# Optimization experiments

Hardware: AMD Instinct MI355X
Metric: run time of the kernel (lower is better)

## Reference

```python
import jax, jax.numpy as jnp
import numpy as np

B, L = 64, 512          # graphs, nodes per graph
N = B * L               # total nodes
INPUT_DIM, D, H, LAYERS, OUT = 128, 128, 8, 6, 10
DH = D // H
FF = 4 * D
E = 4 * N
SCALE = 0.02


def setup_inputs() -> dict:
    key = jax.random.key(0)
    ks = jax.random.split(key, 12)
    p = {}
    p['x'] = jax.random.normal(ks[0], (N, INPUT_DIM), jnp.float32)
    p['edge_index'] = jax.random.randint(ks[1], (2, E), 0, N, dtype=jnp.int64)
    p['batch'] = jnp.repeat(jnp.arange(B, dtype=jnp.int32), L)  # sorted graph ids
    p['max_nodes'] = L
    p['Wp'] = jax.random.normal(ks[2], (INPUT_DIM, D), jnp.float32) * SCALE
    p['bp'] = jnp.zeros((D,), jnp.float32)
    p['qkv_w'] = jax.random.normal(ks[3], (LAYERS, 3 * D, D), jnp.float32) * SCALE
    p['qkv_b'] = jnp.zeros((LAYERS, 3 * D), jnp.float32)
    p['out_w'] = jax.random.normal(ks[4], (LAYERS, D, D), jnp.float32) * SCALE
    p['out_b'] = jnp.zeros((LAYERS, D), jnp.float32)
    p['ln1_g'] = jnp.ones((LAYERS, D), jnp.float32)
    p['ln1_b'] = jnp.zeros((LAYERS, D), jnp.float32)
    p['ffn_w1'] = jax.random.normal(ks[5], (LAYERS, D, FF), jnp.float32) * SCALE
    p['ffn_b1'] = jnp.zeros((LAYERS, FF), jnp.float32)
    p['ffn_w2'] = jax.random.normal(ks[6], (LAYERS, FF, D), jnp.float32) * SCALE
    p['ffn_b2'] = jnp.zeros((LAYERS, D), jnp.float32)
    p['ln2_g'] = jnp.ones((LAYERS, D), jnp.float32)
    p['ln2_b'] = jnp.zeros((LAYERS, D), jnp.float32)
    p['cls_w1'] = jax.random.normal(ks[7], (D, D // 2), jnp.float32) * SCALE
    p['cls_b1'] = jnp.zeros((D // 2,), jnp.float32)
    p['cls_w2'] = jax.random.normal(ks[8], (D // 2, OUT), jnp.float32) * SCALE
    p['cls_b2'] = jnp.zeros((OUT,), jnp.float32)
    return p


def _ln(x, g, b, eps=1e-5):
    m = x.mean(-1, keepdims=True)
    v = ((x - m) ** 2).mean(-1, keepdims=True)
    return (x - m) * jax.lax.rsqrt(v + eps) * g + b


def _forward(x, batch, max_nodes, Wp, bp, qkv_w, qkv_b, out_w, out_b,
             ln1_g, ln1_b, ffn_w1, ffn_b1, ffn_w2, ffn_b2, ln2_g, ln2_b,
             cls_w1, cls_b1, cls_w2, cls_b2):
    n = x.shape[0]
    # --- vectorized ragged-to-dense (replaces the per-graph python loop) ---
    ones = jnp.ones((n,), jnp.int32)
    counts = jax.ops.segment_sum(ones, batch, num_segments=B)          # [B]
    starts = jnp.concatenate([jnp.zeros((1,), jnp.int32), jnp.cumsum(counts)[:-1]])
    pos = jnp.arange(n, dtype=jnp.int32) - starts[batch]               # slot within graph
    h0 = x @ Wp + bp                                                   # [N, D]
    h = jnp.zeros((B, max_nodes, D), h0.dtype).at[batch, pos].set(h0)  # [B, L, D]
    mask = jnp.zeros((B, max_nodes), bool).at[batch, pos].set(True)    # [B, L]
    # additive key-padding bias (src_key_padding_mask=~mask)
    bias = jnp.where(mask, 0.0, -1e9)[:, None, None, :]                # [B,1,1,L]
    inv_sqrt = 1.0 / np.sqrt(DH)
    for i in range(LAYERS):
        # --- post-norm MHA block ---
        qkv = jnp.einsum('bld,ed->ble', h, qkv_w[i]) + qkv_b[i]        # [B,L,3D]
        q, k, v = jnp.split(qkv, 3, axis=-1)
        q = q.reshape(B, max_nodes, H, DH).transpose(0, 2, 1, 3)       # [B,H,L,dh]
        k = k.reshape(B, max_nodes, H, DH).transpose(0, 2, 1, 3)
        v = v.reshape(B, max_nodes, H, DH).transpose(0, 2, 1, 3)
        scores = jnp.einsum('bhqd,bhkd->bhqk', q, k) * inv_sqrt + bias
        attn = jax.nn.softmax(scores, axis=-1)
        o = jnp.einsum('bhqk,bhkd->bhqd', attn, v)                     # [B,H,L,dh]
        o = o.transpose(0, 2, 1, 3).reshape(B, max_nodes, D)
        o = jnp.einsum('bld,ed->ble', o, out_w[i]) + out_b[i]
        h = _ln(h + o, ln1_g[i], ln1_b[i])
        # --- FFN block ---
        ff = jax.nn.relu(h @ ffn_w1[i] + ffn_b1[i]) @ ffn_w2[i] + ffn_b2[i]
        h = _ln(h + ff, ln2_g[i], ln2_b[i])
    # --- masked mean pooling per graph ---
    denom = jnp.maximum(counts.astype(h.dtype), 1.0)[:, None]          # [B,1]
    pooled = (h * mask[..., None].astype(h.dtype)).sum(axis=1) / denom # [B,D]
    # --- classifier head ---
    hid = jax.nn.relu(pooled @ cls_w1 + cls_b1)
    return hid @ cls_w2 + cls_b2                                       # [B,OUT]


def reference(x, edge_index, batch, max_nodes, Wp, bp, qkv_w, qkv_b, out_w, out_b,
              ln1_g, ln1_b, ffn_w1, ffn_b1, ffn_w2, ffn_b2, ln2_g, ln2_b,
              cls_w1, cls_b1, cls_w2, cls_b2):
    # edge_index is accepted (as in the torch module) but never used.
    return _forward(x, batch, max_nodes, Wp, bp, qkv_w, qkv_b, out_w, out_b,
                    ln1_g, ln1_b, ffn_w1, ffn_b1, ffn_w2, ffn_b2, ln2_g, ln2_b,
                    cls_w1, cls_b1, cls_w2, cls_b2)
```

## Files before the change

### kernel.cpp

```cpp
#include <hip/hip_runtime.h>
#include <hip/hip_bf16.h>


#define NROWS (64 * 512)
#define NLAYER 6

typedef __bf16 bf16x8 __attribute__((ext_vector_type(8)));
typedef float  f32x4  __attribute__((ext_vector_type(4)));
typedef float  f32x16 __attribute__((ext_vector_type(16)));

#define QSCALE 0.36067376022224085f

#if defined(__has_builtin)
#  if __has_builtin(__builtin_amdgcn_exp2f)
#    define FAST_EXP2(x) __builtin_amdgcn_exp2f(x)
#  endif
#endif
#ifndef FAST_EXP2
#  define FAST_EXP2(x) __expf((x) * 0.6931471805599453f)
#endif

__device__ __forceinline__ __hip_bfloat16 f2bf(float x) { return __float2bfloat16(x); }

__device__ __forceinline__ __hip_bfloat16 bf_rta(float a) {
  union { float f; unsigned u; } c{a};
  return __builtin_bit_cast(__hip_bfloat16, (unsigned short)((c.u + 0x8000u) >> 16));
}
__device__ __forceinline__ unsigned pk_rta(float a, float b) {
  union { float f; unsigned u; } ca{a}, cb{b};
  return ((ca.u + 0x8000u) >> 16) | ((cb.u + 0x8000u) & 0xFFFF0000u);
}
__device__ __forceinline__ float bf_hi(unsigned u) {
  return __builtin_bit_cast(float, u & 0xFFFF0000u);
}
__device__ __forceinline__ float bf_lo(unsigned u) {
  return __builtin_bit_cast(float, u << 16);
}

#define PN_X   (NROWS * 128)
#define PN_WP  (128 * 128)
#define PN_QW  (6 * 384 * 128)
#define PN_QB  (6 * 384)
#define PN_OW  (6 * 128 * 128)
#define PN_W1  (6 * 128 * 512)
#define PN_W2  (6 * 512 * 128)
#define PB1 PN_X
#define PB2 (PB1 + PN_WP)
#define PB3 (PB2 + PN_QW)
#define PB4 (PB3 + PN_QB)
#define PB5 (PB4 + PN_OW)
#define PB6 (PB5 + PN_W1)
#define PB7 (PB6 + PN_W2)

__global__ __launch_bounds__(256) void prep_kernel(
    const float* __restrict__ x, __hip_bfloat16* __restrict__ xb,
    const float* __restrict__ Wp, __hip_bfloat16* __restrict__ wp_t,
    const float* __restrict__ qkv_w, __hip_bfloat16* __restrict__ qkvw,
    const float* __restrict__ qkv_b, float* __restrict__ qb_s,
    const float* __restrict__ out_w, __hip_bfloat16* __restrict__ outw,
    const float* __restrict__ ffn_w1, __hip_bfloat16* __restrict__ w1t,
    const float* __restrict__ ffn_w2, __hip_bfloat16* __restrict__ w2t)
{
  const int idx = blockIdx.x * 256 + threadIdx.x;
  if (idx < PB1) {
    xb[idx] = f2bf(x[idx]);
  } else if (idx < PB2) {
    const int i = idx - PB1;
    const int c = i >> 7, r = i & 127;
    wp_t[i] = f2bf(Wp[r * 128 + c]);
  } else if (idx < PB3) {
    const int i = idx - PB2;
    const int row = (i >> 7) % 384;
    qkvw[i] = f2bf(qkv_w[i] * ((row < 128) ? QSCALE : 1.f));
  } else if (idx < PB4) {
    const int i = idx - PB3;
    qb_s[i] = qkv_b[i] * (((i % 384) < 128) ? QSCALE : 1.f);
  } else if (idx < PB5) {
    const int i = idx - PB4;
    outw[i] = f2bf(out_w[i]);
  } else if (idx < PB6) {
    const int i = idx - PB5;
    const int l = i >> 16, j = i & 65535;
    const int c = j >> 7, r = j & 127;
    w1t[i] = f2bf(ffn_w1[l * 65536 + r * 512 + c]);
  } else if (idx < PB7) {
    const int i = idx - PB6;
    const int l = i >> 16, j = i & 65535;
    const int c = j >> 9, r = j & 511;
    w2t[i] = f2bf(ffn_w2[l * 65536 + r * 128 + c]);
  }
}

__global__ __launch_bounds__(256) void gemm_fk(
    const __hip_bfloat16* __restrict__ A, const __hip_bfloat16* __restrict__ B,
    const float* __restrict__ bias, __hip_bfloat16* __restrict__ outb,
    __hip_bfloat16* __restrict__ hb,
    const float* __restrict__ lng, const float* __restrict__ lnb,
    int M, int K, int flags)
{
  __shared__ __align__(16) __hip_bfloat16 As[64 * 136];
  __shared__ __align__(16) __hip_bfloat16 Bs[128 * 136];

  const int tid = threadIdx.x;
  const int m0 = blockIdx.x << 6;
  const int wave = tid >> 6;
  const int lane = tid & 63;
  const int quad = lane >> 4;
  const int l15 = lane & 15;
  const int wrow = wave * 16;

  f32x4 acc[8];
#pragma unroll
  for (int ni = 0; ni < 8; ++ni) acc[ni] = (f32x4){0.f, 0.f, 0.f, 0.f};

  for (int kc = 0; kc < K; kc += 128) {
#pragma unroll
    for (int p = 0; p < 4; ++p) {
      const int e = tid + (p << 8);
      const int row = e >> 4;
      const int c = e & 15;
      *(uint4*)&As[row * 136 + c * 8] =
          *(const uint4*)(A + (size_t)(m0 + row) * K + kc + c * 8);
    }
#pragma unroll
    for (int p = 0; p < 8; ++p) {
      const int e = tid + (p << 8);
      const int row = e >> 4;
      const int c = e & 15;
      *(uint4*)&Bs[row * 136 + c * 8] =
          *(const uint4*)(B + (size_t)row * K + kc + c * 8);
    }
    __syncthreads();

#pragma unroll
    for (int ks = 0; ks < 4; ++ks) {
      const bf16x8 af = *(const bf16x8*)&As[(wrow + l15) * 136 + ks * 32 + quad * 8];
#pragma unroll
      for (int ni = 0; ni < 8; ++ni) {
        const bf16x8 bfr =
            *(const bf16x8*)&Bs[(ni * 16 + l15) * 136 + ks * 32 + quad * 8];
        acc[ni] = __builtin_amdgcn_mfma_f32_16x16x32_bf16(af, bfr, acc[ni], 0, 0, 0);
      }
    }
    if (kc + 128 < K) __syncthreads();
  }

  if (flags & 2) {
#pragma unroll
    for (int r = 0; r < 4; ++r) {
      const size_t row = (size_t)(m0 + wrow + quad * 4 + r);
      float s = 0.f, sq = 0.f;
#pragma unroll
      for (int ni = 0; ni < 8; ++ni) {
        const int cl = ni * 16 + l15;
        const float v = acc[ni][r] + bias[cl] +
                        __bfloat162float(hb[row * 128 + cl]);
        acc[ni][r] = v;
        s += v;
        sq += v * v;
      }
#pragma unroll
      for (int off = 1; off <= 8; off <<= 1) {
        s += __shfl_xor(s, off, 64);
        sq += __shfl_xor(sq, off, 64);
      }
      const float mean = s * (1.f / 128.f);
      const float var = sq * (1.f / 128.f) - mean * mean;
      const float rs = rsqrtf(var + 1e-5f);
#pragma unroll
      for (int ni = 0; ni < 8; ++ni) {
        const int cl = ni * 16 + l15;
        const float o = (acc[ni][r] - mean) * rs * lng[cl] + lnb[cl];
        hb[row * 128 + cl] = bf_rta(o);
      }
    }
  } else {
#pragma unroll
    for (int ni = 0; ni < 8; ++ni) {
      const int cl = ni * 16 + l15;
      const float bv = bias[cl];
#pragma unroll
      for (int r = 0; r < 4; ++r) {
        float v = acc[ni][r] + bv;
        if (flags & 1) v = fmaxf(v, 0.f);
        outb[(size_t)(m0 + wrow + quad * 4 + r) * 128 + cl] = bf_rta(v);
      }
    }
  }
}

__global__ __launch_bounds__(256) void oproj_ffn(
    const __hip_bfloat16* __restrict__ ab,
    __hip_bfloat16* __restrict__ hb,
    const __hip_bfloat16* __restrict__ ow,
    const float* __restrict__ ob,
    const float* __restrict__ ln1g, const float* __restrict__ ln1b,
    const __hip_bfloat16* __restrict__ w1,
    const __hip_bfloat16* __restrict__ w2,
    const float* __restrict__ fb1, const float* __restrict__ fb2,
    const float* __restrict__ ln2g, const float* __restrict__ ln2b)
{
  __shared__ __align__(16) __hip_bfloat16 AF[64 * 136];
  __shared__ __align__(16) __hip_bfloat16 Bs[128 * 136];

  const int tid = threadIdx.x;
  const int m0 = blockIdx.x << 6;
  const int wave = tid >> 6;
  const int lane = tid & 63;
  const int quad = lane >> 4;
  const int l15 = lane & 15;
  const int wrow = wave * 16;
  const int node = m0 + wrow + l15;
  const int ch0 = quad * 4;

  uint2 hres[8];
#pragma unroll
  for (int ni = 0; ni < 8; ++ni)
    hres[ni] = *(const uint2*)(hb + (size_t)node * 128 + ni * 16 + ch0);

#pragma unroll
  for (int p = 0; p < 4; ++p) {
    const int e = tid + (p << 8);
    const int row = e >> 4, c = e & 15;
    *(uint4*)&AF[row * 136 + c * 8] =
        *(const uint4*)(ab + (size_t)(m0 + row) * 128 + c * 8);
  }
#pragma unroll
  for (int p = 0; p < 8; ++p) {
    const int e = tid + (p << 8);
    const int row = e >> 4, c = e & 15;
    *(uint4*)&Bs[row * 136 + c * 8] =
        *(const uint4*)(ow + (size_t)row * 128 + c * 8);
  }
  __syncthreads();

  bf16x8 af[4];
#pragma unroll
  for (int ks = 0; ks < 4; ++ks)
    af[ks] = *(const bf16x8*)&AF[(wrow + l15) * 136 + ks * 32 + quad * 8];

  f32x4 acc[8];
#pragma unroll
  for (int ni = 0; ni < 8; ++ni) acc[ni] = (f32x4){0.f, 0.f, 0.f, 0.f};
#pragma unroll
  for (int ks = 0; ks < 4; ++ks)
#pragma unroll
    for (int ni = 0; ni < 8; ++ni) {
      const bf16x8 bfr =
          *(const bf16x8*)&Bs[(ni * 16 + l15) * 136 + ks * 32 + quad * 8];
      acc[ni] = __builtin_amdgcn_mfma_f32_16x16x32_bf16(bfr, af[ks], acc[ni], 0, 0, 0);
    }

  {
    float s = 0.f, sq = 0.f;
#pragma unroll
    for (int ni = 0; ni < 8; ++ni) {
      const f32x4 obv = *(const f32x4*)(ob + ni * 16 + ch0);
#pragma unroll
      for (int r = 0; r < 4; ++r) {
        const unsigned hu = (r & 2) ? hres[ni].y : hres[ni].x;
        const float hv = (r & 1) ? bf_hi(hu) : bf_lo(hu);
        const float v = acc[ni][r] + obv[r] + hv;
        acc[ni][r] = v;
        s += v;
        sq += v * v;
      }
    }
    s += __shfl_xor(s, 16, 64);  sq += __shfl_xor(sq, 16, 64);
    s += __shfl_xor(s, 32, 64);  sq += __shfl_xor(sq, 32, 64);
    const float mean = s * (1.f / 128.f);
    const float rs = rsqrtf(sq * (1.f / 128.f) - mean * mean + 1e-5f);
#pragma unroll
    for (int ni = 0; ni < 8; ++ni) {
      const f32x4 gv = *(const f32x4*)(ln1g + ni * 16 + ch0);
      const f32x4 bv = *(const f32x4*)(ln1b + ni * 16 + ch0);
      const float o0 = (acc[ni][0] - mean) * rs * gv[0] + bv[0];
      const float o1 = (acc[ni][1] - mean) * rs * gv[1] + bv[1];
      const float o2 = (acc[ni][2] - mean) * rs * gv[2] + bv[2];
      const float o3 = (acc[ni][3] - mean) * rs * gv[3] + bv[3];
      const uint2 pk = make_uint2(pk_rta(o0, o1), pk_rta(o2, o3));
      hres[ni] = pk;
      *(uint2*)&AF[(wrow + l15) * 136 + ni * 16 + ch0] = pk;
    }
  }

  __syncthreads();
#pragma unroll
  for (int p = 0; p < 8; ++p) {
    const int e = tid + (p << 8);
    const int row = e >> 4, cc = e & 15;
    *(uint4*)&Bs[row * 136 + cc * 8] =
        *(const uint4*)(w1 + (size_t)row * 128 + cc * 8);
  }
  bf16x8 hf[4];
#pragma unroll
  for (int ks = 0; ks < 4; ++ks)
    hf[ks] = *(const bf16x8*)&AF[(wrow + l15) * 136 + ks * 32 + quad * 8];
  __syncthreads();

  f32x4 facc[8];
#pragma unroll
  for (int ni = 0; ni < 8; ++ni) facc[ni] = (f32x4){0.f, 0.f, 0.f, 0.f};

  for (int c = 0; c < 4; ++c) {
    if (c > 0) {
      __syncthreads();
#pragma unroll
      for (int p = 0; p < 8; ++p) {
        const int e = tid + (p << 8);
        const int row = e >> 4, cc = e & 15;
        *(uint4*)&Bs[row * 136 + cc * 8] =
            *(const uint4*)(w1 + (size_t)(c * 128 + row) * 128 + cc * 8);
      }
      __syncthreads();
    }

    f32x4 fc[8];
#pragma unroll
    for (int ni = 0; ni < 8; ++ni) fc[ni] = (f32x4){0.f, 0.f, 0.f, 0.f};
#pragma unroll
    for (int ks = 0; ks < 4; ++ks)
#pragma unroll
      for (int ni = 0; ni < 8; ++ni) {
        const bf16x8 wf =
            *(const bf16x8*)&Bs[(ni * 16 + l15) * 136 + ks * 32 + quad * 8];
        fc[ni] = __builtin_amdgcn_mfma_f32_16x16x32_bf16(wf, hf[ks], fc[ni], 0, 0, 0);
      }
#pragma unroll
    for (int ni = 0; ni < 8; ++ni) {
      const f32x4 bv = *(const f32x4*)(fb1 + c * 128 + ni * 16 + ch0);
      const float v0 = fmaxf(fc[ni][0] + bv[0], 0.f);
      const float v1 = fmaxf(fc[ni][1] + bv[1], 0.f);
      const float v2 = fmaxf(fc[ni][2] + bv[2], 0.f);
      const float v3 = fmaxf(fc[ni][3] + bv[3], 0.f);
      *(uint2*)&AF[(wrow + l15) * 136 + ni * 16 + ch0] =
          make_uint2(pk_rta(v0, v1), pk_rta(v2, v3));
    }
    __syncthreads();

#pragma unroll
    for (int p = 0; p < 8; ++p) {
      const int e = tid + (p << 8);
      const int row = e >> 4, cc = e & 15;
      *(uint4*)&Bs[row * 136 + cc * 8] =
          *(const uint4*)(w2 + (size_t)row * 512 + c * 128 + cc * 8);
    }
    __syncthreads();

#pragma unroll
    for (int ks2 = 0; ks2 < 4; ++ks2) {
      const bf16x8 ff =
          *(const bf16x8*)&AF[(wrow + l15) * 136 + ks2 * 32 + quad * 8];
#pragma unroll
      for (int ni = 0; ni < 8; ++ni) {
        const bf16x8 wf =
            *(const bf16x8*)&Bs[(ni * 16 + l15) * 136 + ks2 * 32 + quad * 8];
        facc[ni] = __builtin_amdgcn_mfma_f32_16x16x32_bf16(wf, ff, facc[ni], 0, 0, 0);
      }
    }
  }

  {
    float s = 0.f, sq = 0.f;
#pragma unroll
    for (int ni = 0; ni < 8; ++ni) {
      const f32x4 b2v = *(const f32x4*)(fb2 + ni * 16 + ch0);
#pragma unroll
      for (int r = 0; r < 4; ++r) {
        const unsigned hu = (r & 2) ? hres[ni].y : hres[ni].x;
        const float hv = (r & 1) ? bf_hi(hu) : bf_lo(hu);
        const float v = facc[ni][r] + b2v[r] + hv;
        facc[ni][r] = v;
        s += v;
        sq += v * v;
      }
    }
    s += __shfl_xor(s, 16, 64);  sq += __shfl_xor(sq, 16, 64);
    s += __shfl_xor(s, 32, 64);  sq += __shfl_xor(sq, 32, 64);
    const float mean = s * (1.f / 128.f);
    const float rs = rsqrtf(sq * (1.f / 128.f) - mean * mean + 1e-5f);
#pragma unroll
    for (int ni = 0; ni < 8; ++ni) {
      const f32x4 gv = *(const f32x4*)(ln2g + ni * 16 + ch0);
      const f32x4 bv = *(const f32x4*)(ln2b + ni * 16 + ch0);
      const float o0 = (facc[ni][0] - mean) * rs * gv[0] + bv[0];
      const float o1 = (facc[ni][1] - mean) * rs * gv[1] + bv[1];
      const float o2 = (facc[ni][2] - mean) * rs * gv[2] + bv[2];
      const float o3 = (facc[ni][3] - mean) * rs * gv[3] + bv[3];
      *(uint2*)(hb + (size_t)node * 128 + ni * 16 + ch0) =
          make_uint2(pk_rta(o0, o1), pk_rta(o2, o3));
    }
  }
}

__global__ __launch_bounds__(512) void attn_kernel(
    const __hip_bfloat16* __restrict__ hbf,
    const __hip_bfloat16* __restrict__ qkvw_l,
    const float* __restrict__ qb_l,
    __hip_bfloat16* __restrict__ o)
{
  __shared__ __align__(16) __hip_bfloat16 Ks[512 * 24];
  __shared__ __align__(16) __hip_bfloat16 Vt[16 * 520];
  __shared__ __align__(16) __hip_bfloat16 PQ[8][1536];

  const int tid = threadIdx.x;
  const int b = blockIdx.x & 63;
  const int hh = blockIdx.x >> 6;
  const __hip_bfloat16* hrow = hbf + (size_t)b * 512 * 128;

  const int wave = tid >> 6;
  const int lane = tid & 63;
  const int l31 = lane & 31;
  const int l5 = lane >> 5;
  const int l15 = lane & 15;
  const int quad = lane >> 4;
  const int q0 = wave * 64;

  {
    f32x4 qacc[4], kacc[4], vacc[4];
#pragma unroll
    for (int mt = 0; mt < 4; ++mt) {
      qacc[mt] = (f32x4){0.f, 0.f, 0.f, 0.f};
      kacc[mt] = (f32x4){0.f, 0.f, 0.f, 0.f};
      vacc[mt] = (f32x4){0.f, 0.f, 0.f, 0.f};
    }
#pragma unroll
    for (int ks = 0; ks < 4; ++ks) {
      const int kc = ks * 32 + quad * 8;
      const bf16x8 wq = *(const bf16x8*)(qkvw_l + (size_t)(hh * 16 + l15) * 128 + kc);
      const bf16x8 wk = *(const bf16x8*)(qkvw_l + (size_t)(128 + hh * 16 + l15) * 128 + kc);
      const bf16x8 wv = *(const bf16x8*)(qkvw_l + (size_t)(256 + hh * 16 + l15) * 128 + kc);
#pragma unroll
      for (int mt = 0; mt < 4; ++mt) {
        const bf16x8 hf =
            *(const bf16x8*)(hrow + (size_t)(q0 + mt * 16 + l15) * 128 + kc);
        qacc[mt] = __builtin_amdgcn_mfma_f32_16x16x32_bf16(hf, wq, qacc[mt], 0, 0, 0);
        kacc[mt] = __builtin_amdgcn_mfma_f32_16x16x32_bf16(hf, wk, kacc[mt], 0, 0, 0);
        vacc[mt] = __builtin_amdgcn_mfma_f32_16x16x32_bf16(wv, hf, vacc[mt], 0, 0, 0);
      }
    }
    const float qb = qb_l[hh * 16 + l15];
    const float kb = qb_l[128 + hh * 16 + l15];
    const f32x4 vb = *(const f32x4*)(qb_l + 256 + hh * 16 + quad * 4);
#pragma unroll
    for (int mt = 0; mt < 4; ++mt)
#pragma unroll
      for (int r = 0; r < 4; ++r) {
        const int nd = mt * 16 + quad * 4 + r;
        PQ[wave][nd * 24 + l15] = bf_rta(qacc[mt][r] + qb);
        Ks[(q0 + nd) * 24 + l15] = bf_rta(kacc[mt][r] + kb);
        Vt[(quad * 4 + r) * 520 + q0 + mt * 16 + l15] = bf_rta(vacc[mt][r] + vb[r]);
      }
  }

  bf16x8 qf[2];
#pragma unroll
  for (int s = 0; s < 2; ++s)
    qf[s] = *(const bf16x8*)&PQ[wave][(s * 32 + l31) * 24 + l5 * 8];
  __syncthreads();

  __hip_bfloat16* Pw = &PQ[wave][0];
  const f32x16 z16 = {};
  f32x4 oacc[2][2];
#pragma unroll
  for (int s = 0; s < 2; ++s) { oacc[s][0] = (f32x4){0.f,0.f,0.f,0.f};
                                oacc[s][1] = (f32x4){0.f,0.f,0.f,0.f}; }
  float lacc[2] = {0.f, 0.f};

  for (int kt = 0; kt < 16; ++kt) {
    const bf16x8 kf = *(const bf16x8*)&Ks[(kt * 32 + l31) * 24 + l5 * 8];
    const bf16x8 vf = *(const bf16x8*)&Vt[l15 * 520 + kt * 32 + quad * 8];
#pragma unroll
    for (int s = 0; s < 2; ++s) {
      f32x16 st = __builtin_amdgcn_mfma_f32_32x32x16_bf16(kf, qf[s], z16, 0, 0, 0);
      float pr[16];
#pragma unroll
      for (int r = 0; r < 16; ++r) pr[r] = FAST_EXP2(st[r]);
      const float s0 = (pr[0] + pr[1]) + (pr[2] + pr[3]);
      const float s1 = (pr[4] + pr[5]) + (pr[6] + pr[7]);
      const float s2 = (pr[8] + pr[9]) + (pr[10] + pr[11]);
      const float s3 = (pr[12] + pr[13]) + (pr[14] + pr[15]);
      lacc[s] += (s0 + s1) + (s2 + s3);
#pragma unroll
      for (int g = 0; g < 4; ++g) {
        *(uint2*)&Pw[l31 * 40 + g * 8 + l5 * 4] =
            make_uint2(pk_rta(pr[g * 4 + 0], pr[g * 4 + 1]),
                       pk_rta(pr[g * 4 + 2], pr[g * 4 + 3]));
      }
#pragma unroll
      for (int g = 0; g < 2; ++g) {
        const bf16x8 pf = *(const bf16x8*)&Pw[(g * 16 + l15) * 40 + quad * 8];
        oacc[s][g] = __builtin_amdgcn_mfma_f32_16x16x32_bf16(vf, pf, oacc[s][g], 0, 0, 0);
      }
    }
  }

#pragma unroll
  for (int s = 0; s < 2; ++s) {
    const float lv = lacc[s] + __shfl_xor(lacc[s], 32, 64);
#pragma unroll
    for (int g = 0; g < 2; ++g) {
      const float lq = __shfl(lv, g * 16 + l15, 64);
      const float inv = 1.f / lq;
      const int qrow = q0 + s * 32 + g * 16 + l15;
      *(uint2*)(o + ((size_t)b * 512 + qrow) * 128 + hh * 16 + quad * 4) =
          make_uint2(pk_rta(oacc[s][g][0] * inv, oacc[s][g][1] * inv),
                     pk_rta(oacc[s][g][2] * inv, oacc[s][g][3] * inv));
    }
  }
}

__global__ __launch_bounds__(256) void head_kernel(
    const __hip_bfloat16* __restrict__ h,
    const float* __restrict__ w1, const float* __restrict__ b1,
    const float* __restrict__ w2, const float* __restrict__ b2,
    float* __restrict__ out)
{
  __shared__ float part[2][128];
  __shared__ float pooled[128];
  __shared__ float hid[64];

  const int b = blockIdx.x;
  const int tid = threadIdx.x;
  const int d = tid & 127;
  const int half = tid >> 7;

  const __hip_bfloat16* hp = h + ((size_t)b * 512 + (size_t)half * 256) * 128;
  float s = 0.f;
  for (int r = 0; r < 256; ++r) s += __bfloat162float(hp[(size_t)r * 128 + d]);
  part[half][d] = s;
  __syncthreads();

  if (tid < 128) pooled[tid] = (part[0][tid] + part[1][tid]) * (1.f / 512.f);
  __syncthreads();

  if (tid < 64) {
    float a = b1[tid];
    for (int dd = 0; dd < 128; ++dd) a = fmaf(pooled[dd], w1[dd * 64 + tid], a);
    hid[tid] = fmaxf(a, 0.f);
  }
  __syncthreads();

  if (tid < 10) {
    float a = b2[tid];
    for (int j = 0; j < 64; ++j) a = fmaf(hid[j], w2[j * 10 + tid], a);
    out[b * 10 + tid] = a;
  }
}

extern "C" void kernel_launch(void* const* d_in, const int* in_sizes, int n_in,
                              void* d_out, int out_size, void* d_ws, size_t ws_size,
                              hipStream_t stream)
{
  (void)in_sizes; (void)n_in; (void)out_size; (void)ws_size;

  const float* x      = (const float*)d_in[0];
  const float* Wp     = (const float*)d_in[4];
  const float* bp     = (const float*)d_in[5];
  const float* qkv_w  = (const float*)d_in[6];
  const float* qkv_b  = (const float*)d_in[7];
  const float* out_w  = (const float*)d_in[8];
  const float* out_b  = (const float*)d_in[9];
  const float* ln1_g  = (const float*)d_in[10];
  const float* ln1_b  = (const float*)d_in[11];
  const float* ffn_w1 = (const float*)d_in[12];
  const float* ffn_b1 = (const float*)d_in[13];
  const float* ffn_w2 = (const float*)d_in[14];
  const float* ffn_b2 = (const float*)d_in[15];
  const float* ln2_g  = (const float*)d_in[16];
  const float* ln2_b  = (const float*)d_in[17];
  const float* cw1    = (const float*)d_in[18];
  const float* cb1    = (const float*)d_in[19];
  const float* cw2    = (const float*)d_in[20];
  const float* cb2    = (const float*)d_in[21];

  const int N = NROWS;

  __hip_bfloat16* hbf   = (__hip_bfloat16*)d_ws;
  __hip_bfloat16* xb    = hbf + (size_t)N * 128;
  __hip_bfloat16* attnb = xb + (size_t)N * 128;
  __hip_bfloat16* wp_t  = attnb + (size_t)N * 128;
  __hip_bfloat16* qkvw  = wp_t + 128 * 128;
  __hip_bfloat16* outw  = qkvw + 6 * 384 * 128;
  __hip_bfloat16* w1t   = outw + 6 * 128 * 128;
  __hip_bfloat16* w2t   = w1t + 6 * 512 * 128;
  float* qb_s = (float*)(w2t + 6 * 128 * 512);

  const dim3 blk(256);
  __hip_bfloat16* const nob = (__hip_bfloat16*)nullptr;
  const float* const nof = (const float*)nullptr;

  prep_kernel<<<dim3((PB7 + 255) / 256), blk, 0, stream>>>(
      x, xb, Wp, wp_t, qkv_w, qkvw, qkv_b, qb_s, out_w, outw,
      ffn_w1, w1t, ffn_w2, w2t);

  gemm_fk<<<dim3(N / 64), blk, 0, stream>>>(
      xb, wp_t, bp, hbf, nob, nof, nof, N, 128, 0);

  for (int i = 0; i < NLAYER; ++i) {
    attn_kernel<<<dim3(64 * 8), dim3(512), 0, stream>>>(
        hbf, qkvw + (size_t)i * 384 * 128, qb_s + (size_t)i * 384, attnb);

    oproj_ffn<<<dim3(N / 64), blk, 0, stream>>>(
        attnb, hbf,
        outw + (size_t)i * 128 * 128, out_b + (size_t)i * 128,
        ln1_g + (size_t)i * 128, ln1_b + (size_t)i * 128,
        w1t + (size_t)i * 512 * 128, w2t + (size_t)i * 128 * 512,
        ffn_b1 + (size_t)i * 512, ffn_b2 + (size_t)i * 128,
        ln2_g + (size_t)i * 128, ln2_b + (size_t)i * 128);
  }

  head_kernel<<<dim3(64), blk, 0, stream>>>(hbf, cw1, cb1, cw2, cb2, (float*)d_out);
}
```

Before: 491.0 us.

## Prefetch FFN weights into registers and double-buffer attention P tiles

The FFN kernel now loads the attention-output A operand straight from global memory into registers, skipping the LDS round trip. It also prefetches the next W1/W2 weight chunk into registers while the current chunk's MFMAs run, so global loads overlap compute instead of stalling between barriers. The attention kernel double-buffers the per-wave P scratch per s-iteration, changes the row stride from 40 to 36 to alter LDS bank mapping, and raises wave priority around the MFMAs with s_setprio. The trade-off is higher register pressure from the prefetch buffers and more shared memory for the P buffers.

```diff
diff --git a/kernel.cpp b/kernel.cpp
--- a/kernel.cpp
+++ b/kernel.cpp
@@ -213,31 +213,31 @@
   const int node = m0 + wrow + l15;
   const int ch0 = quad * 4;
 
+  const int srow = tid >> 4;
+  const int scol = tid & 15;
+
   uint2 hres[8];
 #pragma unroll
   for (int ni = 0; ni < 8; ++ni)
     hres[ni] = *(const uint2*)(hb + (size_t)node * 128 + ni * 16 + ch0);
-
-#pragma unroll
-  for (int p = 0; p < 4; ++p) {
-    const int e = tid + (p << 8);
-    const int row = e >> 4, c = e & 15;
-    *(uint4*)&AF[row * 136 + c * 8] =
-        *(const uint4*)(ab + (size_t)(m0 + row) * 128 + c * 8);
-  }
+  bf16x8 af[4];
+#pragma unroll
+  for (int ks = 0; ks < 4; ++ks)
+    af[ks] = *(const bf16x8*)(ab + (size_t)node * 128 + ks * 32 + quad * 8);
+
 #pragma unroll
   for (int p = 0; p < 8; ++p) {
-    const int e = tid + (p << 8);
-    const int row = e >> 4, c = e & 15;
-    *(uint4*)&Bs[row * 136 + c * 8] =
-        *(const uint4*)(ow + (size_t)row * 128 + c * 8);
+    const int row = srow + (p << 4);
+    *(uint4*)&Bs[row * 136 + scol * 8] =
+        *(const uint4*)(ow + (size_t)row * 128 + scol * 8);
+  }
+  uint4 pw[8];
+#pragma unroll
+  for (int p = 0; p < 8; ++p) {
+    const int row = srow + (p << 4);
+    pw[p] = *(const uint4*)(w1 + (size_t)row * 128 + scol * 8);
   }
   __syncthreads();
-
-  bf16x8 af[4];
-#pragma unroll
-  for (int ks = 0; ks < 4; ++ks)
-    af[ks] = *(const bf16x8*)&AF[(wrow + l15) * 136 + ks * 32 + quad * 8];
 
   f32x4 acc[8];
 #pragma unroll
@@ -285,12 +285,16 @@
   }
 
   __syncthreads();
+
 #pragma unroll
   for (int p = 0; p < 8; ++p) {
-    const int e = tid + (p << 8);
-    const int row = e >> 4, cc = e & 15;
-    *(uint4*)&Bs[row * 136 + cc * 8] =
-        *(const uint4*)(w1 + (size_t)row * 128 + cc * 8);
+    const int row = srow + (p << 4);
+    *(uint4*)&Bs[row * 136 + scol * 8] = pw[p];
+  }
+#pragma unroll
+  for (int p = 0; p < 8; ++p) {
+    const int row = srow + (p << 4);
+    pw[p] = *(const uint4*)(w2 + (size_t)row * 512 + scol * 8);
   }
   bf16x8 hf[4];
 #pragma unroll
@@ -303,18 +307,6 @@
   for (int ni = 0; ni < 8; ++ni) facc[ni] = (f32x4){0.f, 0.f, 0.f, 0.f};
 
   for (int c = 0; c < 4; ++c) {
-    if (c > 0) {
-      __syncthreads();
-#pragma unroll
-      for (int p = 0; p < 8; ++p) {
-        const int e = tid + (p << 8);
-        const int row = e >> 4, cc = e & 15;
-        *(uint4*)&Bs[row * 136 + cc * 8] =
-            *(const uint4*)(w1 + (size_t)(c * 128 + row) * 128 + cc * 8);
-      }
-      __syncthreads();
-    }
-
     f32x4 fc[8];
 #pragma unroll
     for (int ni = 0; ni < 8; ++ni) fc[ni] = (f32x4){0.f, 0.f, 0.f, 0.f};
@@ -340,10 +332,15 @@
 
 #pragma unroll
     for (int p = 0; p < 8; ++p) {
-      const int e = tid + (p << 8);
-      const int row = e >> 4, cc = e & 15;
-      *(uint4*)&Bs[row * 136 + cc * 8] =
-          *(const uint4*)(w2 + (size_t)row * 512 + c * 128 + cc * 8);
+      const int row = srow + (p << 4);
+      *(uint4*)&Bs[row * 136 + scol * 8] = pw[p];
+    }
+    if (c < 3) {
+#pragma unroll
+      for (int p = 0; p < 8; ++p) {
+        const int row = srow + (p << 4);
+        pw[p] = *(const uint4*)(w1 + (size_t)((c + 1) * 128 + row) * 128 + scol * 8);
+      }
     }
     __syncthreads();
 
@@ -357,6 +354,21 @@
             *(const bf16x8*)&Bs[(ni * 16 + l15) * 136 + ks2 * 32 + quad * 8];
         facc[ni] = __builtin_amdgcn_mfma_f32_16x16x32_bf16(wf, ff, facc[ni], 0, 0, 0);
       }
+    }
+
+    if (c < 3) {
+      __syncthreads();
+#pragma unroll
+      for (int p = 0; p < 8; ++p) {
+        const int row = srow + (p << 4);
+        *(uint4*)&Bs[row * 136 + scol * 8] = pw[p];
+      }
+#pragma unroll
+      for (int p = 0; p < 8; ++p) {
+        const int row = srow + (p << 4);
+        pw[p] = *(const uint4*)(w2 + (size_t)row * 512 + (c + 1) * 128 + scol * 8);
+      }
+      __syncthreads();
     }
   }
 
@@ -393,6 +405,9 @@
   }
 }
 
+#define PSTR 36
+#define PBUF 1152
+
 __global__ __launch_bounds__(512) void attn_kernel(
     const __hip_bfloat16* __restrict__ hbf,
     const __hip_bfloat16* __restrict__ qkvw_l,
@@ -401,7 +416,7 @@
 {
   __shared__ __align__(16) __hip_bfloat16 Ks[512 * 24];
   __shared__ __align__(16) __hip_bfloat16 Vt[16 * 520];
-  __shared__ __align__(16) __hip_bfloat16 PQ[8][1536];
+  __shared__ __align__(16) __hip_bfloat16 PQ[8][2304];
 
   const int tid = threadIdx.x;
   const int b = blockIdx.x & 63;
@@ -459,7 +474,6 @@
     qf[s] = *(const bf16x8*)&PQ[wave][(s * 32 + l31) * 24 + l5 * 8];
   __syncthreads();
 
-  __hip_bfloat16* Pw = &PQ[wave][0];
   const f32x16 z16 = {};
   f32x4 oacc[2][2];
 #pragma unroll
@@ -472,7 +486,10 @@
     const bf16x8 vf = *(const bf16x8*)&Vt[l15 * 520 + kt * 32 + quad * 8];
 #pragma unroll
     for (int s = 0; s < 2; ++s) {
+      __hip_bfloat16* const Pw = &PQ[wave][s * PBUF];
+      __builtin_amdgcn_s_setprio(1);
       f32x16 st = __builtin_amdgcn_mfma_f32_32x32x16_bf16(kf, qf[s], z16, 0, 0, 0);
+      __builtin_amdgcn_s_setprio(0);
       float pr[16];
 #pragma unroll
       for (int r = 0; r < 16; ++r) pr[r] = FAST_EXP2(st[r]);
@@ -483,15 +500,17 @@
       lacc[s] += (s0 + s1) + (s2 + s3);
 #pragma unroll
       for (int g = 0; g < 4; ++g) {
-        *(uint2*)&Pw[l31 * 40 + g * 8 + l5 * 4] =
+        *(uint2*)&Pw[l31 * PSTR + g * 8 + l5 * 4] =
             make_uint2(pk_rta(pr[g * 4 + 0], pr[g * 4 + 1]),
                        pk_rta(pr[g * 4 + 2], pr[g * 4 + 3]));
       }
+      __builtin_amdgcn_s_setprio(1);
 #pragma unroll
       for (int g = 0; g < 2; ++g) {
-        const bf16x8 pf = *(const bf16x8*)&Pw[(g * 16 + l15) * 40 + quad * 8];
+        const bf16x8 pf = *(const bf16x8*)&Pw[(g * 16 + l15) * PSTR + quad * 8];
         oacc[s][g] = __builtin_amdgcn_mfma_f32_16x16x32_bf16(vf, pf, oacc[s][g], 0, 0, 0);
       }
+      __builtin_amdgcn_s_setprio(0);
     }
   }
 
```

Result: slower. 712.4 us (+45.1%).

## Double attention block to 1024 threads with 32 queries per wave and prefetched scores

Applied to the files above, without the earlier changes.

The attention kernel now launches 16 waves per block, each handling 32 query rows instead of 64. This halves per-wave register use and raises in-block parallelism. The K tile drops its padding to a stride of 16 and the Q/P scratch is resized. The next tile's QK^T MFMA is issued before the PV MFMAs of the current tile, so score computation overlaps with softmax and accumulation. Risks are LDS bank conflicts from the unpadded K layout, less reuse of each K/V fragment across queries, and lower occupancy per CU with 1024-thread blocks.

```diff
diff --git a/kernel.cpp b/kernel.cpp
--- a/kernel.cpp
+++ b/kernel.cpp
@@ -393,15 +393,15 @@
   }
 }
 
-__global__ __launch_bounds__(512) void attn_kernel(
+__global__ __launch_bounds__(1024) void attn_kernel(
     const __hip_bfloat16* __restrict__ hbf,
     const __hip_bfloat16* __restrict__ qkvw_l,
     const float* __restrict__ qb_l,
     __hip_bfloat16* __restrict__ o)
 {
-  __shared__ __align__(16) __hip_bfloat16 Ks[512 * 24];
+  __shared__ __align__(16) __hip_bfloat16 Ks[512 * 16];
   __shared__ __align__(16) __hip_bfloat16 Vt[16 * 520];
-  __shared__ __align__(16) __hip_bfloat16 PQ[8][1536];
+  __shared__ __align__(16) __hip_bfloat16 PQ[16][1280];
 
   const int tid = threadIdx.x;
   const int b = blockIdx.x & 63;
@@ -414,12 +414,12 @@
   const int l5 = lane >> 5;
   const int l15 = lane & 15;
   const int quad = lane >> 4;
-  const int q0 = wave * 64;
+  const int q0 = wave * 32;
 
   {
-    f32x4 qacc[4], kacc[4], vacc[4];
-#pragma unroll
-    for (int mt = 0; mt < 4; ++mt) {
+    f32x4 qacc[2], kacc[2], vacc[2];
+#pragma unroll
+    for (int mt = 0; mt < 2; ++mt) {
       qacc[mt] = (f32x4){0.f, 0.f, 0.f, 0.f};
       kacc[mt] = (f32x4){0.f, 0.f, 0.f, 0.f};
       vacc[mt] = (f32x4){0.f, 0.f, 0.f, 0.f};
@@ -431,7 +431,7 @@
       const bf16x8 wk = *(const bf16x8*)(qkvw_l + (size_t)(128 + hh * 16 + l15) * 128 + kc);
       const bf16x8 wv = *(const bf16x8*)(qkvw_l + (size_t)(256 + hh * 16 + l15) * 128 + kc);
 #pragma unroll
-      for (int mt = 0; mt < 4; ++mt) {
+      for (int mt = 0; mt < 2; ++mt) {
         const bf16x8 hf =
             *(const bf16x8*)(hrow + (size_t)(q0 + mt * 16 + l15) * 128 + kc);
         qacc[mt] = __builtin_amdgcn_mfma_f32_16x16x32_bf16(hf, wq, qacc[mt], 0, 0, 0);
@@ -443,70 +443,66 @@
     const float kb = qb_l[128 + hh * 16 + l15];
     const f32x4 vb = *(const f32x4*)(qb_l + 256 + hh * 16 + quad * 4);
 #pragma unroll
-    for (int mt = 0; mt < 4; ++mt)
+    for (int mt = 0; mt < 2; ++mt)
 #pragma unroll
       for (int r = 0; r < 4; ++r) {
         const int nd = mt * 16 + quad * 4 + r;
-        PQ[wave][nd * 24 + l15] = bf_rta(qacc[mt][r] + qb);
-        Ks[(q0 + nd) * 24 + l15] = bf_rta(kacc[mt][r] + kb);
+        PQ[wave][nd * 40 + l15] = bf_rta(qacc[mt][r] + qb);
+        Ks[(q0 + nd) * 16 + l15] = bf_rta(kacc[mt][r] + kb);
         Vt[(quad * 4 + r) * 520 + q0 + mt * 16 + l15] = bf_rta(vacc[mt][r] + vb[r]);
       }
   }
 
-  bf16x8 qf[2];
-#pragma unroll
-  for (int s = 0; s < 2; ++s)
-    qf[s] = *(const bf16x8*)&PQ[wave][(s * 32 + l31) * 24 + l5 * 8];
+  const bf16x8 qf = *(const bf16x8*)&PQ[wave][l31 * 40 + l5 * 8];
   __syncthreads();
 
   __hip_bfloat16* Pw = &PQ[wave][0];
   const f32x16 z16 = {};
-  f32x4 oacc[2][2];
-#pragma unroll
-  for (int s = 0; s < 2; ++s) { oacc[s][0] = (f32x4){0.f,0.f,0.f,0.f};
-                                oacc[s][1] = (f32x4){0.f,0.f,0.f,0.f}; }
-  float lacc[2] = {0.f, 0.f};
+  f32x4 oacc[2];
+  oacc[0] = (f32x4){0.f, 0.f, 0.f, 0.f};
+  oacc[1] = (f32x4){0.f, 0.f, 0.f, 0.f};
+  float lacc = 0.f;
+
+  bf16x8 kf = *(const bf16x8*)&Ks[l31 * 16 + l5 * 8];
+  f32x16 st = __builtin_amdgcn_mfma_f32_32x32x16_bf16(kf, qf, z16, 0, 0, 0);
 
   for (int kt = 0; kt < 16; ++kt) {
-    const bf16x8 kf = *(const bf16x8*)&Ks[(kt * 32 + l31) * 24 + l5 * 8];
     const bf16x8 vf = *(const bf16x8*)&Vt[l15 * 520 + kt * 32 + quad * 8];
-#pragma unroll
-    for (int s = 0; s < 2; ++s) {
-      f32x16 st = __builtin_amdgcn_mfma_f32_32x32x16_bf16(kf, qf[s], z16, 0, 0, 0);
-      float pr[16];
-#pragma unroll
-      for (int r = 0; r < 16; ++r) pr[r] = FAST_EXP2(st[r]);
-      const float s0 = (pr[0] + pr[1]) + (pr[2] + pr[3]);
-      const float s1 = (pr[4] + pr[5]) + (pr[6] + pr[7]);
-      const float s2 = (pr[8] + pr[9]) + (pr[10] + pr[11]);
-      const float s3 = (pr[12] + pr[13]) + (pr[14] + pr[15]);
-      lacc[s] += (s0 + s1) + (s2 + s3);
-#pragma unroll
-      for (int g = 0; g < 4; ++g) {
-        *(uint2*)&Pw[l31 * 40 + g * 8 + l5 * 4] =
-            make_uint2(pk_rta(pr[g * 4 + 0], pr[g * 4 + 1]),
-                       pk_rta(pr[g * 4 + 2], pr[g * 4 + 3]));
-      }
-#pragma unroll
-      for (int g = 0; g < 2; ++g) {
-        const bf16x8 pf = *(const bf16x8*)&Pw[(g * 16 + l15) * 40 + quad * 8];
-        oacc[s][g] = __builtin_amdgcn_mfma_f32_16x16x32_bf16(vf, pf, oacc[s][g], 0, 0, 0);
-      }
-    }
-  }
-
-#pragma unroll
-  for (int s = 0; s < 2; ++s) {
-    const float lv = lacc[s] + __shfl_xor(lacc[s], 32, 64);
+
+    float pr[16];
+#pragma unroll
+    for (int r = 0; r < 16; ++r) pr[r] = FAST_EXP2(st[r]);
+    const float a0 = (pr[0] + pr[1]) + (pr[2] + pr[3]);
+    const float a1 = (pr[4] + pr[5]) + (pr[6] + pr[7]);
+    const float a2 = (pr[8] + pr[9]) + (pr[10] + pr[11]);
+    const float a3 = (pr[12] + pr[13]) + (pr[14] + pr[15]);
+    lacc += (a0 + a1) + (a2 + a3);
+#pragma unroll
+    for (int g = 0; g < 4; ++g) {
+      *(uint2*)&Pw[l31 * 40 + g * 8 + l5 * 4] =
+          make_uint2(pk_rta(pr[g * 4 + 0], pr[g * 4 + 1]),
+                     pk_rta(pr[g * 4 + 2], pr[g * 4 + 3]));
+    }
+    if (kt < 15) {
+      kf = *(const bf16x8*)&Ks[((kt + 1) * 32 + l31) * 16 + l5 * 8];
+      st = __builtin_amdgcn_mfma_f32_32x32x16_bf16(kf, qf, z16, 0, 0, 0);
+    }
 #pragma unroll
     for (int g = 0; g < 2; ++g) {
-      const float lq = __shfl(lv, g * 16 + l15, 64);
-      const float inv = 1.f / lq;
-      const int qrow = q0 + s * 32 + g * 16 + l15;
-      *(uint2*)(o + ((size_t)b * 512 + qrow) * 128 + hh * 16 + quad * 4) =
-          make_uint2(pk_rta(oacc[s][g][0] * inv, oacc[s][g][1] * inv),
-                     pk_rta(oacc[s][g][2] * inv, oacc[s][g][3] * inv));
-    }
+      const bf16x8 pf = *(const bf16x8*)&Pw[(g * 16 + l15) * 40 + quad * 8];
+      oacc[g] = __builtin_amdgcn_mfma_f32_16x16x32_bf16(vf, pf, oacc[g], 0, 0, 0);
+    }
+  }
+
+  const float lv = lacc + __shfl_xor(lacc, 32, 64);
+#pragma unroll
+  for (int g = 0; g < 2; ++g) {
+    const float lq = __shfl(lv, g * 16 + l15, 64);
+    const float inv = 1.f / lq;
+    const int qrow = q0 + g * 16 + l15;
+    *(uint2*)(o + ((size_t)b * 512 + qrow) * 128 + hh * 16 + quad * 4) =
+        make_uint2(pk_rta(oacc[g][0] * inv, oacc[g][1] * inv),
+                   pk_rta(oacc[g][2] * inv, oacc[g][3] * inv));
   }
 }
 
@@ -598,7 +594,7 @@
       xb, wp_t, bp, hbf, nob, nof, nof, N, 128, 0);
 
   for (int i = 0; i < NLAYER; ++i) {
-    attn_kernel<<<dim3(64 * 8), dim3(512), 0, stream>>>(
+    attn_kernel<<<dim3(64 * 8), dim3(1024), 0, stream>>>(
         hbf, qkvw + (size_t)i * 384 * 128, qb_s + (size_t)i * 384, attnb);
 
     oproj_ffn<<<dim3(N / 64), blk, 0, stream>>>(
```

Result: slower. 516.5 us (+5.2%).
